# Kernel optimization log

Measured on AMD Instinct MI355X. Metric: run time of the kernel, lower is better.

Reference implementation:

```python
import jax, jax.numpy as jnp
import numpy as np

WS = 8          # window size
SHIFT = WS // 2 # cyclic shift for shifted windows
HEADS = 6
C = 192
EMB = 256
HID = 4 * C
EPS = 1e-5


def _inorm(x):
    # InstanceNorm2d (affine=False): normalize each (sample, channel) over spatial dims
    m = x.mean(axis=(2, 3), keepdims=True)
    v = x.var(axis=(2, 3), keepdims=True)
    return (x - m) * jax.lax.rsqrt(v + EPS)


def _rel_index(ws):
    c = jnp.stack(jnp.meshgrid(jnp.arange(ws), jnp.arange(ws), indexing='ij'), -1).reshape(-1, 2)
    r = c[:, None] - c[None, :] + (ws - 1)          # (N,N,2) in [0, 2ws-2]
    return r[..., 0] * (2 * ws - 1) + r[..., 1]     # (N,N)


def _attn_mask(H, W, ws, shift):
    # standard Swin shifted-window mask: tokens from different pre-shift regions can't attend
    def ids(L):
        a = jnp.arange(L)
        return (a >= L - ws).astype(jnp.int32) + (a >= L - shift).astype(jnp.int32)
    img = ids(H)[:, None] * 3 + ids(W)[None, :]                     # (H,W)
    imgw = img.reshape(H // ws, ws, W // ws, ws).transpose(0, 2, 1, 3).reshape(-1, ws * ws)  # (nW,N)
    return jnp.where(imgw[:, None, :] != imgw[:, :, None], -1e9, 0.0)  # (nW,N,N)


def setup_inputs() -> dict:
    key = jax.random.key(0)
    ks = jax.random.split(key, 12)
    s = 0.02
    return {
        'x':        jax.random.normal(ks[0], (8, C, 128, 128), jnp.float32),
        'cond':     jax.random.normal(ks[1], (8, EMB), jnp.float32),
        'qkv_w':    jax.random.normal(ks[2], (3 * C, C), jnp.float32) * s,
        'qkv_b':    jnp.zeros((3 * C,), jnp.float32),
        'proj_w':   jax.random.normal(ks[3], (C, C), jnp.float32) * s,
        'proj_b':   jnp.zeros((C,), jnp.float32),
        'rel_bias': jax.random.normal(ks[4], ((2 * WS - 1) ** 2, HEADS), jnp.float32) * s,
        'film_w':   jax.random.normal(ks[5], (2 * C, EMB), jnp.float32) * s,
        'film_b':   jnp.zeros((2 * C,), jnp.float32),
        'mlp_w1':   jax.random.normal(ks[6], (HID, C), jnp.float32) * s,
        'mlp_b1':   jnp.zeros((HID,), jnp.float32),
        'mlp_w2':   jax.random.normal(ks[7], (C, HID), jnp.float32) * s,
        'mlp_b2':   jnp.zeros((C,), jnp.float32),
    }


def reference(x, cond, qkv_w, qkv_b, proj_w, proj_b, rel_bias,
              film_w, film_b, mlp_w1, mlp_b1, mlp_w2, mlp_b2):
    B, Cc, H, W = x.shape
    N = WS * WS
    nW = (H // WS) * (W // WS)
    hd = Cc // HEADS

    # ---- x = x + attn(norm1(x)) : shifted window attention ----
    xn = _inorm(x)
    xs = jnp.roll(xn, (-SHIFT, -SHIFT), axis=(2, 3))
    # window partition -> (B, nW, N, C)
    xw = (xs.reshape(B, Cc, H // WS, WS, W // WS, WS)
            .transpose(0, 2, 4, 3, 5, 1)
            .reshape(B, nW, N, Cc))
    qkv = xw @ qkv_w.T + qkv_b                       # (B,nW,N,3C)
    q, k, v = jnp.split(qkv, 3, axis=-1)
    def heads(t):
        return t.reshape(B, nW, N, HEADS, hd).transpose(0, 1, 3, 2, 4)  # (B,nW,H,N,hd)
    q, k, v = heads(q), heads(k), heads(v)
    attn = jnp.einsum('bwhnd,bwhmd->bwhnm', q, k) * (hd ** -0.5)
    bias = rel_bias[_rel_index(WS)].transpose(2, 0, 1)   # (HEADS,N,N)
    mask = _attn_mask(H, W, WS, SHIFT)                   # (nW,N,N)
    attn = attn + bias[None, None] + mask[None, :, None]
    a = jax.nn.softmax(attn, axis=-1)
    o = jnp.einsum('bwhnm,bwhmd->bwhnd', a, v)
    o = o.transpose(0, 1, 3, 2, 4).reshape(B, nW, N, Cc)
    o = o @ proj_w.T + proj_b
    # window reverse -> (B,C,H,W), undo shift
    o = (o.reshape(B, H // WS, W // WS, WS, WS, Cc)
           .transpose(0, 5, 1, 3, 2, 4)
           .reshape(B, Cc, H, W))
    o = jnp.roll(o, (SHIFT, SHIFT), axis=(2, 3))
    x = x + o

    # ---- x = x + mlp(FiLM(norm2(x), cond)) ----
    h = _inorm(x)
    gb = cond @ film_w.T + film_b                     # (B,2C)
    scale, shift = gb[:, :Cc], gb[:, Cc:]
    h = h * (1.0 + scale)[:, :, None, None] + shift[:, :, None, None]
    h = jnp.einsum('bchw,oc->bohw', h, mlp_w1) + mlp_b1[None, :, None, None]
    h = jax.nn.gelu(h, approximate=True)              # GELU('tanh')
    h = jnp.einsum('bchw,oc->bohw', h, mlp_w2) + mlp_b2[None, :, None, None]
    return x + h
```

## Files before the change

kernel.cpp:

```cpp
#include <hip/hip_runtime.h>
#include <hip/hip_bf16.h>

using bf16 = __hip_bfloat16;

#define HEADS 6
#define EPSV 1e-5f
#define QS 0.17677669529663687f

typedef __bf16 bfv8 __attribute__((ext_vector_type(8)));
typedef short sv8 __attribute__((ext_vector_type(8)));
typedef float fv4 __attribute__((ext_vector_type(4)));

__device__ __forceinline__ unsigned short f2bfbits(float f) {
  union { float f; unsigned u; } x{f};
  unsigned r = x.u + 0x7fffu + ((x.u >> 16) & 1u);
  return (unsigned short)(r >> 16);
}

__device__ __forceinline__ int swz(int row, int col, int rowstride) {
  return row * rowstride + ((((col >> 3) ^ (row & 7)) << 3) | (col & 7));
}

__device__ __forceinline__ int swz32(int row, int col) {
  return row * 32 + ((((col >> 3) ^ ((row >> 1) & 3)) << 3) | (col & 7));
}

__device__ __forceinline__ uint2 pack4b(fv4 a, float b0, float b1, float b2, float b3) {
  uint2 r;
  r.x = (unsigned)f2bfbits(a[0] + b0) | ((unsigned)f2bfbits(a[1] + b1) << 16);
  r.y = (unsigned)f2bfbits(a[2] + b2) | ((unsigned)f2bfbits(a[3] + b3) << 16);
  return r;
}

template <bool BW>
__device__ __forceinline__ bfv8 ldwf(const short* wb, const float* wf, int row,
                                     int k, int ld, float scale) {
  if constexpr (BW) {
    return *(const bfv8*)(wb + (size_t)row * ld + k);
  } else {
    const float* p = wf + (size_t)row * ld + k;
    float4 a = *(const float4*)p;
    float4 b = *(const float4*)(p + 4);
    sv8 s;
    s[0] = (short)f2bfbits(a.x * scale); s[1] = (short)f2bfbits(a.y * scale);
    s[2] = (short)f2bfbits(a.z * scale); s[3] = (short)f2bfbits(a.w * scale);
    s[4] = (short)f2bfbits(b.x * scale); s[5] = (short)f2bfbits(b.y * scale);
    s[6] = (short)f2bfbits(b.z * scale); s[7] = (short)f2bfbits(b.w * scale);
    return __builtin_bit_cast(bfv8, s);
  }
}

__device__ __forceinline__ void stats_body(const float* __restrict__ x, int bc,
                                           float2* __restrict__ mr, int tid) {
  const float4* p = (const float4*)(x + (size_t)bc * 16384);
  float s = 0.f, s2 = 0.f;
  for (int i = tid; i < 4096; i += 256) {
    float4 v = p[i];
    s += v.x + v.y + v.z + v.w;
    s2 = fmaf(v.x, v.x, s2);
    s2 = fmaf(v.y, v.y, s2);
    s2 = fmaf(v.z, v.z, s2);
    s2 = fmaf(v.w, v.w, s2);
  }
#pragma unroll
  for (int off = 32; off > 0; off >>= 1) {
    s += __shfl_down(s, off);
    s2 += __shfl_down(s2, off);
  }
  __shared__ float rs[4], rs2[4];
  int wid = tid >> 6;
  if ((tid & 63) == 0) { rs[wid] = s; rs2[wid] = s2; }
  __syncthreads();
  if (tid == 0) {
    float S = rs[0] + rs[1] + rs[2] + rs[3];
    float S2 = rs2[0] + rs2[1] + rs2[2] + rs2[3];
    float m = S * (1.f / 16384.f);
    float v = S2 * (1.f / 16384.f) - m * m;
    mr[bc] = make_float2(m, rsqrtf(v + EPSV));
  }
}

__global__ __launch_bounds__(256) void stats_kernel(const float* __restrict__ x,
                                                    float2* __restrict__ mr) {
  stats_body(x, blockIdx.x, mr, threadIdx.x);
}

__device__ __forceinline__ void pack8(float4 a, float4 b, float sc, short* dst) {
  uint4 o;
  o.x = (unsigned)f2bfbits(a.x * sc) | ((unsigned)f2bfbits(a.y * sc) << 16);
  o.y = (unsigned)f2bfbits(a.z * sc) | ((unsigned)f2bfbits(a.w * sc) << 16);
  o.z = (unsigned)f2bfbits(b.x * sc) | ((unsigned)f2bfbits(b.y * sc) << 16);
  o.w = (unsigned)f2bfbits(b.z * sc) | ((unsigned)f2bfbits(b.w * sc) << 16);
  *(uint4*)dst = o;
}

__global__ __launch_bounds__(256) void fused_pre_kernel(
    const float* __restrict__ x, float2* __restrict__ mr1,
    const float* __restrict__ cond, const float* __restrict__ fw,
    const float* __restrict__ fb, float* __restrict__ gb,
    const float* __restrict__ qkv_w, const float* __restrict__ proj_w,
    const float* __restrict__ mlp_w1, const float* __restrict__ mlp_w2,
    short* __restrict__ wbA, int nUnits) {
  int bid = blockIdx.x;
  if (bid < 1536) {
    stats_body(x, bid, mr1, threadIdx.x);
    return;
  }
  bid -= 1536;
  if (bid < 12) {
    int g = bid * 256 + threadIdx.x;
    if (g >= 8 * 384) return;
    int b = g / 384, o = g % 384;
    const float* c = cond + b * 256;
    const float* w = fw + o * 256;
    float acc = fb[o];
    for (int k = 0; k < 256; k += 4) {
      float4 cv = *(const float4*)(c + k);
      float4 wv = *(const float4*)(w + k);
      acc = fmaf(cv.x, wv.x, acc);
      acc = fmaf(cv.y, wv.y, acc);
      acc = fmaf(cv.z, wv.z, acc);
      acc = fmaf(cv.w, wv.w, acc);
    }
    gb[g] = acc;
    return;
  }
  int u = (bid - 12) * 256 + threadIdx.x;
  if (u >= nUnits) return;
  if (u < 18432) {
    int e = u * 8;
    float sc = (e < 36864) ? QS : 1.f;
    const float* src = (e < 110592) ? (qkv_w + e) : (proj_w + (e - 110592));
    pack8(*(const float4*)src, *(const float4*)(src + 4), sc, wbA + e);
  } else if (u < 36864) {
    int f = (u - 18432) * 8;
    int ob = f / 12288, s = f % 12288;
    int row = s / 192, within = s % 192;
    int col0 = (((within >> 3) ^ (row & 7)) << 3);
    const float* src = mlp_w1 + (size_t)(ob * 64 + row) * 192 + col0;
    pack8(*(const float4*)src, *(const float4*)(src + 4), 1.f, wbA + 147456 + f);
  } else {
    int f = (u - 36864) * 8;
    int chunk = f / 6144, s = f % 6144;
    int r = s / 32, within = s % 32;
    int blk = within >> 3;
    int ob = chunk >> 1, ch = chunk & 1;
    int srccol = ob * 64 + ch * 32 + ((blk ^ ((r >> 1) & 3)) << 3);
    const float* src = mlp_w2 + (size_t)r * 768 + srccol;
    pack8(*(const float4*)src, *(const float4*)(src + 4), 1.f, wbA + 294912 + f);
  }
}

template <bool BW>
__global__ __launch_bounds__(512, 4) void attn_mfma5_kernel(
    const float* __restrict__ x, const float2* __restrict__ mr1,
    const short* __restrict__ wb, const float* __restrict__ qkv_w,
    const float* __restrict__ qkv_b, const float* __restrict__ proj_w,
    const float* __restrict__ proj_b, const float* __restrict__ rel_bias,
    float* __restrict__ out) {
  __shared__ __align__(16) short s_x[64 * 192];
  __shared__ __align__(16) short s_k[64 * 192];
  __shared__ __align__(16) short s_v[192 * 64];
  __shared__ float s_rel[1350];

  const short* wbq = wb;
  const short* wbp = wb + 110592;

  int tid = threadIdx.x;
  int blk = ((blockIdx.x & 7) << 8) + (blockIdx.x >> 3);
  int b = blk >> 8;
  int wdw = blk & 255;
  int wh = wdw >> 4, ww = wdw & 15;
  int lane = tid & 63;
  int w = tid >> 6;
  int nloc = lane & 15, lg = lane >> 4;

  for (int i = tid; i < 1350; i += 512) s_rel[i] = rel_bias[i];

  for (int u = tid; u < 3072; u += 512) {
    int jh = u & 1, ii = (u >> 1) & 7, c = u >> 4;
    int hg = (wh * 8 + ii + 4) & 127;
    int wc0 = (ww * 8 + jh * 4 + 4) & 127;
    float4 v = *(const float4*)&x[((size_t)(b * 192 + c) << 14) + (hg << 7) + wc0];
    float2 mrv = mr1[b * 192 + c];
    int n0 = ii * 8 + jh * 4;
    s_x[swz(n0 + 0, c, 192)] = (short)f2bfbits((v.x - mrv.x) * mrv.y);
    s_x[swz(n0 + 1, c, 192)] = (short)f2bfbits((v.y - mrv.x) * mrv.y);
    s_x[swz(n0 + 2, c, 192)] = (short)f2bfbits((v.z - mrv.x) * mrv.y);
    s_x[swz(n0 + 3, c, 192)] = (short)f2bfbits((v.w - mrv.x) * mrv.y);
  }
  __syncthreads();

  for (int half = 0; half < 2; half++) {
    int ptb = half * 2;
    bfv8 xf[2][6];
#pragma unroll
    for (int pp = 0; pp < 2; pp++)
#pragma unroll
      for (int ks = 0; ks < 6; ks++)
        xf[pp][ks] = *(const bfv8*)&s_x[swz((ptb + pp) * 16 + nloc, ks * 32 + lg * 8, 192)];
    __syncthreads();

    for (int t = w; t < 36; t += 8) {
      bool isQK = (t < 24);
      int baserow = isQK ? t * 16 : 384 + (t - 24) * 16;
      float scl = (!BW && t < 12) ? QS : 1.f;
      bfv8 wf[6];
#pragma unroll
      for (int ks = 0; ks < 6; ks++)
        wf[ks] = ldwf<BW>(wbq, qkv_w, baserow + nloc, ks * 32 + lg * 8, 192, scl);
      __builtin_amdgcn_s_setprio(1);
#pragma unroll
      for (int pp = 0; pp < 2; pp++) {
        int pt = ptb + pp;
        fv4 acc = fv4{0.f, 0.f, 0.f, 0.f};
        if (isQK) {
#pragma unroll
          for (int ks = 0; ks < 6; ks++)
            acc = __builtin_amdgcn_mfma_f32_16x16x32_bf16(wf[ks], xf[pp][ks], acc, 0, 0, 0);
          int o0 = t * 16 + lg * 4;
          float4 bb = *(const float4*)&qkv_b[o0];
          float bsc = (t < 12) ? QS : 1.f;
          uint2 pkk = pack4b(acc, bb.x * bsc, bb.y * bsc, bb.z * bsc, bb.w * bsc);
          if (t < 12)
            *(uint2*)&s_x[swz(pt * 16 + nloc, o0, 192)] = pkk;
          else
            *(uint2*)&s_k[swz(pt * 16 + nloc, o0 - 192, 192)] = pkk;
        } else {
#pragma unroll
          for (int ks = 0; ks < 6; ks++)
            acc = __builtin_amdgcn_mfma_f32_16x16x32_bf16(xf[pp][ks], wf[ks], acc, 0, 0, 0);
          int d = (t - 24) * 16 + nloc;
          float bv = qkv_b[384 + d];
          *(uint2*)&s_v[swz(d, pt * 16 + lg * 4, 64)] = pack4b(acc, bv, bv, bv, bv);
        }
      }
      __builtin_amdgcn_s_setprio(0);
    }
  }
  __syncthreads();

  int maskh = (wh == 15), maskw = (ww == 15);
#pragma unroll
  for (int ui = 0; ui < 3; ui++) {
    int u = w * 3 + ui;
    int hh = u >> 2, ng = u & 3;
    int n = ng * 16 + nloc;
    int i1 = n >> 3, j1 = n & 7;
    int gn = (maskh ? (i1 < 4 ? 1 : 2) : 0) * 3 + (maskw ? (j1 < 4 ? 1 : 2) : 0);

    bfv8 qf = *(const bfv8*)&s_x[swz(n, hh * 32 + lg * 8, 192)];
    fv4 sc[4];
    __builtin_amdgcn_s_setprio(1);
#pragma unroll
    for (int mt = 0; mt < 4; mt++) {
      bfv8 kf = *(const bfv8*)&s_k[swz(mt * 16 + nloc, hh * 32 + lg * 8, 192)];
      sc[mt] = __builtin_amdgcn_mfma_f32_16x16x32_bf16(kf, qf, fv4{0.f, 0.f, 0.f, 0.f}, 0, 0, 0);
    }
    __builtin_amdgcn_s_setprio(0);
    float vals[16];
#pragma unroll
    for (int mt = 0; mt < 4; mt++) {
#pragma unroll
      for (int r = 0; r < 4; r++) {
        int m = mt * 16 + lg * 4 + r;
        int i2 = m >> 3, j2 = m & 7;
        int gm = (maskh ? (i2 < 4 ? 1 : 2) : 0) * 3 + (maskw ? (j2 < 4 ? 1 : 2) : 0);
        float v = sc[mt][r] + s_rel[((i1 - i2 + 7) * 15 + (j1 - j2 + 7)) * 6 + hh];
        vals[mt * 4 + r] = (gn == gm) ? v : v - 1e9f;
      }
    }
    float mx = vals[0];
#pragma unroll
    for (int q = 1; q < 16; q++) mx = fmaxf(mx, vals[q]);
    mx = fmaxf(mx, __shfl_xor(mx, 16));
    mx = fmaxf(mx, __shfl_xor(mx, 32));
    float sum = 0.f;
#pragma unroll
    for (int q = 0; q < 16; q++) {
      vals[q] = __expf(vals[q] - mx);
      sum += vals[q];
    }
    sum += __shfl_xor(sum, 16);
    sum += __shfl_xor(sum, 32);
    float inv = 1.f / sum;

    unsigned pk[4][2];
#pragma unroll
    for (int mt = 0; mt < 4; mt++) {
      pk[mt][0] = (unsigned)f2bfbits(vals[mt * 4] * inv) |
                  ((unsigned)f2bfbits(vals[mt * 4 + 1] * inv) << 16);
      pk[mt][1] = (unsigned)f2bfbits(vals[mt * 4 + 2] * inv) |
                  ((unsigned)f2bfbits(vals[mt * 4 + 3] * inv) << 16);
    }
    int sel = lg >> 1;
    int S0 = nloc + ((lg & 1) << 5);
    int S1 = S0 + 16;
    bfv8 pf[2];
#pragma unroll
    for (int ks = 0; ks < 2; ks++) {
      unsigned a0 = (unsigned)__shfl((int)pk[2 * ks][0], S0);
      unsigned b0 = (unsigned)__shfl((int)pk[2 * ks + 1][0], S0);
      unsigned a1 = (unsigned)__shfl((int)pk[2 * ks][1], S0);
      unsigned b1 = (unsigned)__shfl((int)pk[2 * ks + 1][1], S0);
      unsigned a2 = (unsigned)__shfl((int)pk[2 * ks][0], S1);
      unsigned b2 = (unsigned)__shfl((int)pk[2 * ks + 1][0], S1);
      unsigned a3 = (unsigned)__shfl((int)pk[2 * ks][1], S1);
      unsigned b3 = (unsigned)__shfl((int)pk[2 * ks + 1][1], S1);
      uint4 uu;
      uu.x = sel ? b0 : a0;
      uu.y = sel ? b1 : a1;
      uu.z = sel ? b2 : a2;
      uu.w = sel ? b3 : a3;
      pf[ks] = __builtin_bit_cast(bfv8, uu);
    }
    __builtin_amdgcn_s_setprio(1);
#pragma unroll
    for (int dt = 0; dt < 2; dt++) {
      fv4 oa = fv4{0.f, 0.f, 0.f, 0.f};
#pragma unroll
      for (int ks = 0; ks < 2; ks++) {
        bfv8 vf = *(const bfv8*)&s_v[swz(hh * 32 + dt * 16 + nloc, ks * 32 + lg * 8, 64)];
        oa = __builtin_amdgcn_mfma_f32_16x16x32_bf16(vf, pf[ks], oa, 0, 0, 0);
      }
      int d0 = hh * 32 + dt * 16 + lg * 4;
      *(uint2*)&s_x[swz(n, d0, 192)] = pack4b(oa, 0.f, 0.f, 0.f, 0.f);
    }
    __builtin_amdgcn_s_setprio(0);
  }
  __syncthreads();

  {
    int a2 = w >> 1, half = w & 1;
#pragma unroll
    for (int ci = 0; ci < 3; ci++) {
      int ct = a2 * 3 + ci;
      bfv8 wf[6];
#pragma unroll
      for (int ks = 0; ks < 6; ks++)
        wf[ks] = ldwf<BW>(wbp, proj_w, ct * 16 + nloc, ks * 32 + lg * 8, 192, 1.f);
#pragma unroll
      for (int ni = 0; ni < 2; ni++) {
        int nt = half * 2 + ni;
        fv4 acc = fv4{0.f, 0.f, 0.f, 0.f};
        __builtin_amdgcn_s_setprio(1);
#pragma unroll
        for (int ks = 0; ks < 6; ks++) {
          bfv8 of = *(const bfv8*)&s_x[swz(nt * 16 + nloc, ks * 32 + lg * 8, 192)];
          acc = __builtin_amdgcn_mfma_f32_16x16x32_bf16(wf[ks], of, acc, 0, 0, 0);
        }
        __builtin_amdgcn_s_setprio(0);
        int n = nt * 16 + nloc;
        int ii = n >> 3, jj = n & 7;
        int hg = (wh * 8 + ii + 4) & 127;
        int wc = (ww * 8 + jj + 4) & 127;
        float4 pb4 = *(const float4*)&proj_b[ct * 16 + lg * 4];
        const float* pbp = &pb4.x;
#pragma unroll
        for (int r = 0; r < 4; r++) {
          int c = ct * 16 + lg * 4 + r;
          size_t gi = ((size_t)(b * 192 + c) << 14) + (hg << 7) + wc;
          out[gi] = x[gi] + acc[r] + pbp[r];
        }
      }
    }
  }
}

__global__ __launch_bounds__(512, 2) void mlp_mfma5_kernel(
    float* __restrict__ xio, const float2* __restrict__ mr2,
    const float* __restrict__ gb, const short* __restrict__ w1s,
    const short* __restrict__ w2s, const float* __restrict__ b1,
    const float* __restrict__ b2) {
  __shared__ __align__(16) short s_pool[2 * 12288];
  __shared__ __align__(16) short s_h[128 * 32];
  __shared__ float s_b1[768];
  __shared__ float s_mean[192], s_rstd[192], s_scale[192], s_shift[192], s_b2[192];

  int tid = threadIdx.x;
  int blk = blockIdx.x;
  int b = blk >> 7;
  int p0 = (blk & 127) << 7;
  int lane = tid & 63;
  int w = tid >> 6;

  for (int i = tid; i < 768; i += 512) s_b1[i] = b1[i];
  for (int i = tid; i < 192; i += 512) {
    float2 mrv = mr2[b * 192 + i];
    s_mean[i] = mrv.x;
    s_rstd[i] = mrv.y;
    s_scale[i] = 1.f + gb[b * 384 + i];
    s_shift[i] = gb[b * 384 + 192 + i];
    s_b2[i] = b2[i];
  }
  __syncthreads();

  for (int e = tid; e < 768; e += 512) {
    int pq = e & 31, cb = e >> 5;
    int p = pq * 4, c0 = cb * 8;
    float4 xv[8];
#pragma unroll
    for (int j = 0; j < 8; j++)
      xv[j] = *(const float4*)&xio[((size_t)(b * 192 + c0 + j) << 14) + p0 + p];
#pragma unroll
    for (int j = 0; j < 8; j++) {
      int c = c0 + j;
      float mn = s_mean[c], rs = s_rstd[c], scv = s_scale[c], sh = s_shift[c];
      xv[j].x = (xv[j].x - mn) * rs * scv + sh;
      xv[j].y = (xv[j].y - mn) * rs * scv + sh;
      xv[j].z = (xv[j].z - mn) * rs * scv + sh;
      xv[j].w = (xv[j].w - mn) * rs * scv + sh;
    }
#pragma unroll
    for (int pp = 0; pp < 4; pp++) {
      sv8 pk;
#pragma unroll
      for (int j = 0; j < 8; j++) pk[j] = (short)f2bfbits((&xv[j].x)[pp]);
      *(sv8*)&s_pool[swz(p + pp, c0, 192)] = pk;
    }
  }
  __syncthreads();

  int prow = w * 16 + (lane & 15);
  bfv8 afr[6];
#pragma unroll
  for (int ks = 0; ks < 6; ks++) {
    int c = ks * 32 + (lane >> 4) * 8;
    afr[ks] = *(const bfv8*)&s_pool[swz(prow, c, 192)];
  }
  __syncthreads();

  char* poolBytes = (char*)s_pool;
  const char* w1B = (const char*)w1s;
  const char* w2B = (const char*)w2s;

  fv4 acc2[12];
#pragma unroll
  for (int i = 0; i < 12; i++) acc2[i] = fv4{0.f, 0.f, 0.f, 0.f};

#define STAGE_HALF(hb, bufIdx)                                                        \
  {                                                                                   \
    char* dstB = poolBytes + (bufIdx)*24576;                                          \
    _Pragma("unroll") for (int j = 0; j < 3; j++) {                                   \
      int ch = w * 3 + j;                                                             \
      const char* srcB = (ch < 12) ? (w1B + (size_t)(hb)*12288 + ch * 1024)           \
                                   : (w2B + (size_t)(hb)*12288 + (ch - 12) * 1024);   \
      __builtin_amdgcn_global_load_lds(                                               \
          (const __attribute__((address_space(1))) void*)(srcB + lane * 16),          \
          (__attribute__((address_space(3))) void*)(dstB + ch * 1024), 16, 0, 0);     \
    }                                                                                 \
  }

  STAGE_HALF(0, 0);
  asm volatile("s_waitcnt vmcnt(0)" ::: "memory");
  __builtin_amdgcn_s_barrier();

  for (int i = 0; i < 24; ++i) {
    int cur = i & 1;
    if (i < 23) STAGE_HALF(i + 1, cur ^ 1);

    const short* bw1 = s_pool + cur * 12288;
    const short* bw2 = s_pool + cur * 12288 + 6144;

#pragma unroll
    for (int it = 0; it < 2; it++) {
      fv4 a1 = fv4{0.f, 0.f, 0.f, 0.f};
      int orow = it * 16 + (lane & 15);
      __builtin_amdgcn_s_setprio(1);
#pragma unroll
      for (int ks = 0; ks < 6; ks++) {
        int c = ks * 32 + (lane >> 4) * 8;
        bfv8 wf = *(const bfv8*)&bw1[swz(orow, c, 192)];
        a1 = __builtin_amdgcn_mfma_f32_16x16x32_bf16(wf, afr[ks], a1, 0, 0, 0);
      }
      __builtin_amdgcn_s_setprio(0);
      int o0 = i * 32 + it * 16 + (lane >> 4) * 4;
      unsigned short hbv[4];
#pragma unroll
      for (int r = 0; r < 4; r++) {
        float v = a1[r] + s_b1[o0 + r];
        float g = v / (1.f + __expf(-1.5957691216f * fmaf(0.044715f * v * v, v, v)));
        hbv[r] = f2bfbits(g);
      }
      uint2 pk;
      pk.x = (unsigned)hbv[0] | ((unsigned)hbv[1] << 16);
      pk.y = (unsigned)hbv[2] | ((unsigned)hbv[3] << 16);
      int ol = it * 16 + (lane >> 4) * 4;
      *(uint2*)&s_h[swz32(prow, ol)] = pk;
    }

    bfv8 hf = *(const bfv8*)&s_h[swz32(prow, (lane >> 4) * 8)];
    __builtin_amdgcn_s_setprio(1);
#pragma unroll
    for (int it2 = 0; it2 < 12; it2++) {
      int crow = it2 * 16 + (lane & 15);
      bfv8 w2f = *(const bfv8*)&bw2[swz32(crow, (lane >> 4) * 8)];
      acc2[it2] = __builtin_amdgcn_mfma_f32_16x16x32_bf16(w2f, hf, acc2[it2], 0, 0, 0);
    }
    __builtin_amdgcn_s_setprio(0);

    if (i < 23) {
      asm volatile("s_waitcnt vmcnt(0)" ::: "memory");
      __builtin_amdgcn_s_barrier();
    }
  }
#undef STAGE_HALF

  int p = p0 + w * 16 + (lane & 15);
#pragma unroll
  for (int it2 = 0; it2 < 12; it2++) {
    int c0 = it2 * 16 + (lane >> 4) * 4;
#pragma unroll
    for (int r = 0; r < 4; r++) {
      int c = c0 + r;
      size_t gi = ((size_t)(b * 192 + c) << 14) + p;
      xio[gi] += acc2[it2][r] + s_b2[c];
    }
  }
}

__global__ __launch_bounds__(512, 2) void mlp_mfma_kernel(
    float* __restrict__ xio, const float2* __restrict__ mr2,
    const float* __restrict__ gb, const float* __restrict__ w1,
    const float* __restrict__ b1, const float* __restrict__ w2,
    const float* __restrict__ b2) {
  __shared__ __align__(16) short s_a[128 * 192];
  __shared__ __align__(16) short s_h[128 * 64];
  __shared__ __align__(16) short s_w1[64 * 192];
  __shared__ __align__(16) short s_w2[192 * 64];
  __shared__ float s_b1[768];
  __shared__ float s_mean[192], s_rstd[192], s_scale[192], s_shift[192], s_b2[192];

  int tid = threadIdx.x;
  int blk = blockIdx.x;
  int b = blk >> 7;
  int p0 = (blk & 127) << 7;
  int lane = tid & 63;
  int w = tid >> 6;

  for (int i = tid; i < 768; i += 512) s_b1[i] = b1[i];
  for (int i = tid; i < 192; i += 512) {
    float2 mrv = mr2[b * 192 + i];
    s_mean[i] = mrv.x;
    s_rstd[i] = mrv.y;
    s_scale[i] = 1.f + gb[b * 384 + i];
    s_shift[i] = gb[b * 384 + 192 + i];
    s_b2[i] = b2[i];
  }
  __syncthreads();

  for (int e = tid; e < 3072; e += 512) {
    int p = e & 127, cb = e >> 7;
    int c0 = cb * 8;
    sv8 pk;
#pragma unroll
    for (int j = 0; j < 8; j++) {
      int c = c0 + j;
      float xv = xio[((size_t)(b * 192 + c) << 14) + p0 + p];
      float hn = (xv - s_mean[c]) * s_rstd[c];
      pk[j] = (short)f2bfbits(hn * s_scale[c] + s_shift[c]);
    }
    *(sv8*)&s_a[swz(p, c0, 192)] = pk;
  }
  __syncthreads();

  int prow = w * 16 + (lane & 15);
  bfv8 afr[6];
#pragma unroll
  for (int ks = 0; ks < 6; ks++) {
    int c = ks * 32 + (lane >> 4) * 8;
    afr[ks] = *(const bfv8*)&s_a[swz(prow, c, 192)];
  }

  fv4 acc2[12];
#pragma unroll
  for (int i = 0; i < 12; i++) acc2[i] = fv4{0.f, 0.f, 0.f, 0.f};

  for (int ob = 0; ob < 12; ob++) {
    __syncthreads();
    for (int e = tid; e < 3072; e += 512) {
      int row = e / 48, ch4 = e % 48;
      float4 v = *(const float4*)&w1[(size_t)(ob * 64 + row) * 192 + ch4 * 4];
      uint2 pk;
      pk.x = (unsigned)f2bfbits(v.x) | ((unsigned)f2bfbits(v.y) << 16);
      pk.y = (unsigned)f2bfbits(v.z) | ((unsigned)f2bfbits(v.w) << 16);
      *(uint2*)&s_w1[swz(row, ch4 * 4, 192)] = pk;
    }
    for (int e = tid; e < 3072; e += 512) {
      int row = e >> 4, o4 = (e & 15) * 4;
      float4 v = *(const float4*)&w2[(size_t)row * 768 + ob * 64 + o4];
      uint2 pk;
      pk.x = (unsigned)f2bfbits(v.x) | ((unsigned)f2bfbits(v.y) << 16);
      pk.y = (unsigned)f2bfbits(v.z) | ((unsigned)f2bfbits(v.w) << 16);
      *(uint2*)&s_w2[swz(row, o4, 64)] = pk;
    }
    __syncthreads();

#pragma unroll
    for (int it = 0; it < 4; it++) {
      fv4 a1 = fv4{0.f, 0.f, 0.f, 0.f};
      int orow = it * 16 + (lane & 15);
#pragma unroll
      for (int ks = 0; ks < 6; ks++) {
        int c = ks * 32 + (lane >> 4) * 8;
        bfv8 wf = *(const bfv8*)&s_w1[swz(orow, c, 192)];
        a1 = __builtin_amdgcn_mfma_f32_16x16x32_bf16(wf, afr[ks], a1, 0, 0, 0);
      }
      int o0 = ob * 64 + it * 16 + (lane >> 4) * 4;
      unsigned short hb[4];
#pragma unroll
      for (int r = 0; r < 4; r++) {
        float v = a1[r] + s_b1[o0 + r];
        float g = v / (1.f + __expf(-1.5957691216f * fmaf(0.044715f * v * v, v, v)));
        hb[r] = f2bfbits(g);
      }
      uint2 pk;
      pk.x = (unsigned)hb[0] | ((unsigned)hb[1] << 16);
      pk.y = (unsigned)hb[2] | ((unsigned)hb[3] << 16);
      int ol = it * 16 + (lane >> 4) * 4;
      *(uint2*)&s_h[swz(prow, ol, 64)] = pk;
    }

#pragma unroll
    for (int ks2 = 0; ks2 < 2; ks2++) {
      int ol = ks2 * 32 + (lane >> 4) * 8;
      bfv8 hf = *(const bfv8*)&s_h[swz(prow, ol, 64)];
#pragma unroll
      for (int it2 = 0; it2 < 12; it2++) {
        int crow = it2 * 16 + (lane & 15);
        bfv8 w2f = *(const bfv8*)&s_w2[swz(crow, ol, 64)];
        acc2[it2] = __builtin_amdgcn_mfma_f32_16x16x32_bf16(w2f, hf, acc2[it2], 0, 0, 0);
      }
    }
  }

  int p = p0 + w * 16 + (lane & 15);
#pragma unroll
  for (int it2 = 0; it2 < 12; it2++) {
    int c0 = it2 * 16 + (lane >> 4) * 4;
#pragma unroll
    for (int r = 0; r < 4; r++) {
      int c = c0 + r;
      size_t gi = ((size_t)(b * 192 + c) << 14) + p;
      xio[gi] += acc2[it2][r] + s_b2[c];
    }
  }
}

extern "C" void kernel_launch(void* const* d_in, const int* in_sizes, int n_in,
                              void* d_out, int out_size, void* d_ws, size_t ws_size,
                              hipStream_t stream) {
  const float* x = (const float*)d_in[0];
  const float* cond = (const float*)d_in[1];
  const float* qkv_w = (const float*)d_in[2];
  const float* qkv_b = (const float*)d_in[3];
  const float* proj_w = (const float*)d_in[4];
  const float* proj_b = (const float*)d_in[5];
  const float* rel_bias = (const float*)d_in[6];
  const float* film_w = (const float*)d_in[7];
  const float* film_b = (const float*)d_in[8];
  const float* mlp_w1 = (const float*)d_in[9];
  const float* mlp_b1 = (const float*)d_in[10];
  const float* mlp_w2 = (const float*)d_in[11];
  const float* mlp_b2 = (const float*)d_in[12];

  float* out = (float*)d_out;
  char* wsb = (char*)d_ws;

  float2* mr1 = (float2*)wsb;
  float2* mr2 = (float2*)(wsb + 12288);
  float* gb = (float*)(wsb + 24576);
  const size_t base = 36864;
  const size_t wbB = 442368ull * 2;
  short* wbA = (short*)(wsb + base);

  bool haveA = ws_size >= base + 294912;
  bool haveM = ws_size >= base + wbB;

  int nUnits = haveM ? 55296 : (haveA ? 18432 : 0);
  fused_pre_kernel<<<1536 + 12 + (nUnits + 255) / 256, 256, 0, stream>>>(
      x, mr1, cond, film_w, film_b, gb, qkv_w, proj_w, mlp_w1, mlp_w2, wbA, nUnits);

  if (haveA)
    attn_mfma5_kernel<true><<<2048, 512, 0, stream>>>(
        x, mr1, wbA, qkv_w, qkv_b, proj_w, proj_b, rel_bias, out);
  else
    attn_mfma5_kernel<false><<<2048, 512, 0, stream>>>(
        x, mr1, wbA, qkv_w, qkv_b, proj_w, proj_b, rel_bias, out);

  stats_kernel<<<1536, 256, 0, stream>>>(out, mr2);

  if (haveM)
    mlp_mfma5_kernel<<<1024, 512, 0, stream>>>(out, mr2, gb, wbA + 147456,
                                               wbA + 294912, mlp_b1, mlp_b2);
  else
    mlp_mfma_kernel<<<1024, 512, 0, stream>>>(out, mr2, gb, mlp_w1, mlp_b1,
                                              mlp_w2, mlp_b2);
}
```

Measured before the change: 382.0 us.

## Keep V in registers, store relative bias as bf16 to cut LDS footprint

The V projection is now computed by each wave only for the heads it later consumes and kept in registers, then redistributed with lane shuffles. This removes the s_v shared buffer. The relative-position bias table is stored as bf16, weight fragments are streamed per k-step instead of preloaded, and launch bounds drop from 4 to 3 blocks per CU. The aim is to cut LDS usage and LDS traffic, at the cost of recomputing V tiles shared by waves, adding shuffle work and rounding the bias to bf16.

```diff
diff --git a/kernel.cpp b/kernel.cpp
--- a/kernel.cpp
+++ b/kernel.cpp
@@ -152,7 +152,7 @@
 }
 
 template <bool BW>
-__global__ __launch_bounds__(512, 4) void attn_mfma5_kernel(
+__global__ __launch_bounds__(512, 3) void attn_mfma6_kernel(
     const float* __restrict__ x, const float2* __restrict__ mr1,
     const short* __restrict__ wb, const float* __restrict__ qkv_w,
     const float* __restrict__ qkv_b, const float* __restrict__ proj_w,
@@ -160,8 +160,7 @@
     float* __restrict__ out) {
   __shared__ __align__(16) short s_x[64 * 192];
   __shared__ __align__(16) short s_k[64 * 192];
-  __shared__ __align__(16) short s_v[192 * 64];
-  __shared__ float s_rel[1350];
+  __shared__ short s_relb[1350];
 
   const short* wbq = wb;
   const short* wbp = wb + 110592;
@@ -175,7 +174,11 @@
   int w = tid >> 6;
   int nloc = lane & 15, lg = lane >> 4;
 
-  for (int i = tid; i < 1350; i += 512) s_rel[i] = rel_bias[i];
+  int hh_lo = (3 * w) >> 2;
+  int hh_hi = (3 * w + 2) >> 2;
+  int nvt = (hh_hi != hh_lo) ? 4 : 2;
+
+  for (int i = tid; i < 1350; i += 512) s_relb[i] = (short)f2bfbits(rel_bias[i]);
 
   for (int u = tid; u < 3072; u += 512) {
     int jh = u & 1, ii = (u >> 1) & 7, c = u >> 4;
@@ -191,6 +194,8 @@
   }
   __syncthreads();
 
+  uint2 vpk[4][4];
+
   for (int half = 0; half < 2; half++) {
     int ptb = half * 2;
     bfv8 xf[2][6];
@@ -201,41 +206,50 @@
         xf[pp][ks] = *(const bfv8*)&s_x[swz((ptb + pp) * 16 + nloc, ks * 32 + lg * 8, 192)];
     __syncthreads();
 
-    for (int t = w; t < 36; t += 8) {
-      bool isQK = (t < 24);
-      int baserow = isQK ? t * 16 : 384 + (t - 24) * 16;
-      float scl = (!BW && t < 12) ? QS : 1.f;
-      bfv8 wf[6];
-#pragma unroll
-      for (int ks = 0; ks < 6; ks++)
-        wf[ks] = ldwf<BW>(wbq, qkv_w, baserow + nloc, ks * 32 + lg * 8, 192, scl);
+    for (int t = w; t < 24; t += 8) {
+      bool isQ = (t < 12);
+      float scl = (!BW && isQ) ? QS : 1.f;
+      fv4 acc0 = fv4{0.f, 0.f, 0.f, 0.f};
+      fv4 acc1 = fv4{0.f, 0.f, 0.f, 0.f};
       __builtin_amdgcn_s_setprio(1);
 #pragma unroll
-      for (int pp = 0; pp < 2; pp++) {
-        int pt = ptb + pp;
-        fv4 acc = fv4{0.f, 0.f, 0.f, 0.f};
-        if (isQK) {
-#pragma unroll
-          for (int ks = 0; ks < 6; ks++)
-            acc = __builtin_amdgcn_mfma_f32_16x16x32_bf16(wf[ks], xf[pp][ks], acc, 0, 0, 0);
-          int o0 = t * 16 + lg * 4;
-          float4 bb = *(const float4*)&qkv_b[o0];
-          float bsc = (t < 12) ? QS : 1.f;
-          uint2 pkk = pack4b(acc, bb.x * bsc, bb.y * bsc, bb.z * bsc, bb.w * bsc);
-          if (t < 12)
-            *(uint2*)&s_x[swz(pt * 16 + nloc, o0, 192)] = pkk;
-          else
-            *(uint2*)&s_k[swz(pt * 16 + nloc, o0 - 192, 192)] = pkk;
-        } else {
-#pragma unroll
-          for (int ks = 0; ks < 6; ks++)
-            acc = __builtin_amdgcn_mfma_f32_16x16x32_bf16(xf[pp][ks], wf[ks], acc, 0, 0, 0);
-          int d = (t - 24) * 16 + nloc;
-          float bv = qkv_b[384 + d];
-          *(uint2*)&s_v[swz(d, pt * 16 + lg * 4, 64)] = pack4b(acc, bv, bv, bv, bv);
-        }
+      for (int ks = 0; ks < 6; ks++) {
+        bfv8 wf = ldwf<BW>(wbq, qkv_w, t * 16 + nloc, ks * 32 + lg * 8, 192, scl);
+        acc0 = __builtin_amdgcn_mfma_f32_16x16x32_bf16(wf, xf[0][ks], acc0, 0, 0, 0);
+        acc1 = __builtin_amdgcn_mfma_f32_16x16x32_bf16(wf, xf[1][ks], acc1, 0, 0, 0);
       }
       __builtin_amdgcn_s_setprio(0);
+      int o0 = t * 16 + lg * 4;
+      float4 bb = *(const float4*)&qkv_b[o0];
+      float bsc = isQ ? QS : 1.f;
+      uint2 pk0 = pack4b(acc0, bb.x * bsc, bb.y * bsc, bb.z * bsc, bb.w * bsc);
+      uint2 pk1 = pack4b(acc1, bb.x * bsc, bb.y * bsc, bb.z * bsc, bb.w * bsc);
+      if (isQ) {
+        *(uint2*)&s_x[swz(ptb * 16 + nloc, o0, 192)] = pk0;
+        *(uint2*)&s_x[swz((ptb + 1) * 16 + nloc, o0, 192)] = pk1;
+      } else {
+        *(uint2*)&s_k[swz(ptb * 16 + nloc, o0 - 192, 192)] = pk0;
+        *(uint2*)&s_k[swz((ptb + 1) * 16 + nloc, o0 - 192, 192)] = pk1;
+      }
+    }
+
+#pragma unroll
+    for (int vt = 0; vt < 4; vt++) {
+      if (vt >= nvt) break;
+      int T = 2 * hh_lo + vt;
+      fv4 acc0 = fv4{0.f, 0.f, 0.f, 0.f};
+      fv4 acc1 = fv4{0.f, 0.f, 0.f, 0.f};
+      __builtin_amdgcn_s_setprio(1);
+#pragma unroll
+      for (int ks = 0; ks < 6; ks++) {
+        bfv8 wfv = ldwf<BW>(wbq, qkv_w, 384 + T * 16 + nloc, ks * 32 + lg * 8, 192, 1.f);
+        acc0 = __builtin_amdgcn_mfma_f32_16x16x32_bf16(xf[0][ks], wfv, acc0, 0, 0, 0);
+        acc1 = __builtin_amdgcn_mfma_f32_16x16x32_bf16(xf[1][ks], wfv, acc1, 0, 0, 0);
+      }
+      __builtin_amdgcn_s_setprio(0);
+      float bv = qkv_b[384 + T * 16 + nloc];
+      vpk[vt][ptb] = pack4b(acc0, bv, bv, bv, bv);
+      vpk[vt][ptb + 1] = pack4b(acc1, bv, bv, bv, bv);
     }
   }
   __syncthreads();
@@ -266,7 +280,10 @@
         int m = mt * 16 + lg * 4 + r;
         int i2 = m >> 3, j2 = m & 7;
         int gm = (maskh ? (i2 < 4 ? 1 : 2) : 0) * 3 + (maskw ? (j2 < 4 ? 1 : 2) : 0);
-        float v = sc[mt][r] + s_rel[((i1 - i2 + 7) * 15 + (j1 - j2 + 7)) * 6 + hh];
+        unsigned rb = (unsigned)(unsigned short)
+                          s_relb[((i1 - i2 + 7) * 15 + (j1 - j2 + 7)) * 6 + hh]
+                      << 16;
+        float v = sc[mt][r] + __uint_as_float(rb);
         vals[mt * 4 + r] = (gn == gm) ? v : v - 1e9f;
       }
     }
@@ -314,15 +331,37 @@
       uu.w = sel ? b3 : a3;
       pf[ks] = __builtin_bit_cast(bfv8, uu);
     }
+    bool hiv = (hh != hh_lo);
+    bfv8 vf[2][2];
+#pragma unroll
+    for (int dt = 0; dt < 2; dt++) {
+#pragma unroll
+      for (int ks = 0; ks < 2; ks++) {
+        uint2 cA = hiv ? vpk[2 + dt][2 * ks] : vpk[dt][2 * ks];
+        uint2 cB = hiv ? vpk[2 + dt][2 * ks + 1] : vpk[dt][2 * ks + 1];
+        unsigned a0 = (unsigned)__shfl((int)cA.x, S0);
+        unsigned b0 = (unsigned)__shfl((int)cB.x, S0);
+        unsigned a1 = (unsigned)__shfl((int)cA.y, S0);
+        unsigned b1 = (unsigned)__shfl((int)cB.y, S0);
+        unsigned a2 = (unsigned)__shfl((int)cA.x, S1);
+        unsigned b2 = (unsigned)__shfl((int)cB.x, S1);
+        unsigned a3 = (unsigned)__shfl((int)cA.y, S1);
+        unsigned b3 = (unsigned)__shfl((int)cB.y, S1);
+        uint4 uu;
+        uu.x = sel ? b0 : a0;
+        uu.y = sel ? b1 : a1;
+        uu.z = sel ? b2 : a2;
+        uu.w = sel ? b3 : a3;
+        vf[dt][ks] = __builtin_bit_cast(bfv8, uu);
+      }
+    }
     __builtin_amdgcn_s_setprio(1);
 #pragma unroll
     for (int dt = 0; dt < 2; dt++) {
       fv4 oa = fv4{0.f, 0.f, 0.f, 0.f};
 #pragma unroll
-      for (int ks = 0; ks < 2; ks++) {
-        bfv8 vf = *(const bfv8*)&s_v[swz(hh * 32 + dt * 16 + nloc, ks * 32 + lg * 8, 64)];
-        oa = __builtin_amdgcn_mfma_f32_16x16x32_bf16(vf, pf[ks], oa, 0, 0, 0);
-      }
+      for (int ks = 0; ks < 2; ks++)
+        oa = __builtin_amdgcn_mfma_f32_16x16x32_bf16(vf[dt][ks], pf[ks], oa, 0, 0, 0);
       int d0 = hh * 32 + dt * 16 + lg * 4;
       *(uint2*)&s_x[swz(n, d0, 192)] = pack4b(oa, 0.f, 0.f, 0.f, 0.f);
     }
@@ -335,10 +374,6 @@
 #pragma unroll
     for (int ci = 0; ci < 3; ci++) {
       int ct = a2 * 3 + ci;
-      bfv8 wf[6];
-#pragma unroll
-      for (int ks = 0; ks < 6; ks++)
-        wf[ks] = ldwf<BW>(wbp, proj_w, ct * 16 + nloc, ks * 32 + lg * 8, 192, 1.f);
 #pragma unroll
       for (int ni = 0; ni < 2; ni++) {
         int nt = half * 2 + ni;
@@ -346,8 +381,9 @@
         __builtin_amdgcn_s_setprio(1);
 #pragma unroll
         for (int ks = 0; ks < 6; ks++) {
+          bfv8 wf = ldwf<BW>(wbp, proj_w, ct * 16 + nloc, ks * 32 + lg * 8, 192, 1.f);
           bfv8 of = *(const bfv8*)&s_x[swz(nt * 16 + nloc, ks * 32 + lg * 8, 192)];
-          acc = __builtin_amdgcn_mfma_f32_16x16x32_bf16(wf[ks], of, acc, 0, 0, 0);
+          acc = __builtin_amdgcn_mfma_f32_16x16x32_bf16(wf, of, acc, 0, 0, 0);
         }
         __builtin_amdgcn_s_setprio(0);
         int n = nt * 16 + nloc;
@@ -682,10 +718,10 @@
       x, mr1, cond, film_w, film_b, gb, qkv_w, proj_w, mlp_w1, mlp_w2, wbA, nUnits);
 
   if (haveA)
-    attn_mfma5_kernel<true><<<2048, 512, 0, stream>>>(
+    attn_mfma6_kernel<true><<<2048, 512, 0, stream>>>(
         x, mr1, wbA, qkv_w, qkv_b, proj_w, proj_b, rel_bias, out);
   else
-    attn_mfma5_kernel<false><<<2048, 512, 0, stream>>>(
+    attn_mfma6_kernel<false><<<2048, 512, 0, stream>>>(
         x, mr1, wbA, qkv_w, qkv_b, proj_w, proj_b, rel_bias, out);
 
   stats_kernel<<<1536, 256, 0, stream>>>(out, mr2);
```

After: 459.3 us. 1.2x slower.
